# Optimization experiments

Hardware: AMD Instinct MI355X
Metric: run time of the kernel (lower is better)

The kernel has to match this reference:

```python
import jax, jax.numpy as jnp
import numpy as np

H = 1024
V = 50257
L = 512


def setup_inputs() -> dict:
    key = jax.random.key(0)
    ks = jax.random.split(key, 12)
    s = 0.02
    return {
        "input_tok": jax.random.randint(ks[0], (1,), 0, V, dtype=jnp.int64),
        "hidden": jax.random.normal(ks[1], (1, 1, H), dtype=jnp.float32),
        "encoder_outputs": jax.random.normal(ks[2], (L, 1, H), dtype=jnp.float32),
        "embedding_w": jax.random.normal(ks[3], (V, H), dtype=jnp.float32) * s,
        "attn_combine_w": jax.random.normal(ks[4], (H, 2 * H), dtype=jnp.float32) * s,
        "attn_combine_b": jax.random.normal(ks[5], (H,), dtype=jnp.float32) * s,
        "w_ih": jax.random.normal(ks[6], (3 * H, H), dtype=jnp.float32) * s,
        "w_hh": jax.random.normal(ks[7], (3 * H, H), dtype=jnp.float32) * s,
        "b_ih": jax.random.normal(ks[8], (3 * H,), dtype=jnp.float32) * s,
        "b_hh": jax.random.normal(ks[9], (3 * H,), dtype=jnp.float32) * s,
        "out_w": jax.random.normal(ks[10], (V, H), dtype=jnp.float32) * s,
        "out_b": jax.random.normal(ks[11], (V,), dtype=jnp.float32) * s,
    }


def reference(input_tok, hidden, encoder_outputs, embedding_w,
              attn_combine_w, attn_combine_b, w_ih, w_hh, b_ih, b_hh,
              out_w, out_b):
    # embedding(input).view(1,1,-1); dropout is identity in eval mode
    embedded = embedding_w[input_tok[0]][None, :]          # [1, H]
    enc = encoder_outputs[:, 0, :]                          # [L, H]
    h0 = hidden[0]                                          # [1, H]
    # dot-product attention: hidden[0] @ enc^T
    attn_weights = jax.nn.softmax(h0 @ enc.T, axis=1)      # [1, L]
    attn_applied = attn_weights @ enc                       # [1, H]
    combined = jnp.concatenate([embedded, attn_applied], axis=1)  # [1, 2H]
    x = jax.nn.relu(combined @ attn_combine_w.T + attn_combine_b)  # [1, H]
    # single-step GRU cell (PyTorch gate ordering: r, z, n)
    gi = x @ w_ih.T + b_ih                                  # [1, 3H]
    gh = h0 @ w_hh.T + b_hh                                 # [1, 3H]
    r = jax.nn.sigmoid(gi[:, :H] + gh[:, :H])
    z = jax.nn.sigmoid(gi[:, H:2 * H] + gh[:, H:2 * H])
    n = jnp.tanh(gi[:, 2 * H:] + r * gh[:, 2 * H:])
    h_new = (1.0 - z) * n + z * h0                          # [1, H]
    logp = jax.nn.log_softmax(h_new @ out_w.T + out_b, axis=1)  # [1, V]
    return logp, h_new[None], attn_weights
```

## Files before the change

kernel.cpp:

```cpp
#include <hip/hip_runtime.h>
#include <math.h>

#define H   1024
#define H2  2048
#define V   50257
#define L   512
#define NL  3142
#define NAB 16

__device__ __forceinline__ float dot4(float4 a, float4 b) {
    return a.x*b.x + a.y*b.y + a.z*b.z + a.w*b.w;
}
__device__ __forceinline__ float wave_red_sum(float v) {
    #pragma unroll
    for (int off = 32; off > 0; off >>= 1) v += __shfl_down(v, off, 64);
    return v;
}
__device__ __forceinline__ float wave_red_max(float v) {
    #pragma unroll
    for (int off = 32; off > 0; off >>= 1) v = fmaxf(v, __shfl_down(v, off, 64));
    return v;
}

__global__ void __launch_bounds__(256) k_scores(
        const float* __restrict__ h0, const float* __restrict__ enc,
        float* __restrict__ scores) {
    __shared__ float sred[4];
    int t = threadIdx.x, lane = t & 63, wv = t >> 6;
    int l = blockIdx.x;
    float4 a = ((const float4*)(enc + (size_t)l * H))[t];
    float4 b = ((const float4*)h0)[t];
    float acc = wave_red_sum(dot4(a, b));
    if (lane == 0) sred[wv] = acc;
    __syncthreads();
    if (t == 0) scores[l] = sred[0] + sred[1] + sred[2] + sred[3];
}

__global__ void __launch_bounds__(256) k_attn_part(
        const float* __restrict__ enc, const float* __restrict__ scores,
        float* __restrict__ partial, float* __restrict__ d_out) {
    __shared__ float wl[L];
    __shared__ float sred[4];
    int t = threadIdx.x, lane = t & 63, wv = t >> 6;
    float s0 = scores[t], s1 = scores[t + 256];
    float m = wave_red_max(fmaxf(s0, s1));
    if (lane == 0) sred[wv] = m;
    __syncthreads();
    float gmax = fmaxf(fmaxf(sred[0], sred[1]), fmaxf(sred[2], sred[3]));
    __syncthreads();
    float e0 = expf(s0 - gmax), e1 = expf(s1 - gmax);
    float ssum = wave_red_sum(e0 + e1);
    if (lane == 0) sred[wv] = ssum;
    __syncthreads();
    float inv = 1.f / (sred[0] + sred[1] + sred[2] + sred[3]);
    float w0 = e0 * inv, w1 = e1 * inv;
    wl[t] = w0; wl[t + 256] = w1;
    if (blockIdx.x == 0) {
        d_out[V + H + t]       = w0;
        d_out[V + H + 256 + t] = w1;
    }
    __syncthreads();
    int r0 = blockIdx.x * 32;
    float4 acc = make_float4(0.f, 0.f, 0.f, 0.f);
    #pragma unroll 8
    for (int k = 0; k < 32; ++k) {
        float w  = wl[r0 + k];
        float4 e = ((const float4*)(enc + (size_t)(r0 + k) * H))[t];
        acc.x += w * e.x; acc.y += w * e.y; acc.z += w * e.z; acc.w += w * e.w;
    }
    ((float4*)(partial + (size_t)blockIdx.x * H))[t] = acc;
}

__global__ void __launch_bounds__(256) k_combine(
        const float* __restrict__ emb_w, const int* __restrict__ tok,
        const float* __restrict__ partial, const float* __restrict__ Wc,
        const float* __restrict__ bc, float* __restrict__ x) {
    __shared__ float comb[H2];
    int t = threadIdx.x;
    float4 a = make_float4(0.f, 0.f, 0.f, 0.f);
    #pragma unroll
    for (int b = 0; b < NAB; ++b) {
        float4 p = ((const float4*)(partial + (size_t)b * H))[t];
        a.x += p.x; a.y += p.y; a.z += p.z; a.w += p.w;
    }
    int tk = tok[0];
    ((float4*)comb)[t]       = ((const float4*)(emb_w + (size_t)tk * H))[t];
    ((float4*)comb)[t + 256] = a;
    __syncthreads();
    int lane = t & 63, wv = t >> 6;
    int row = blockIdx.x * 4 + wv;
    const float4* wr = (const float4*)(Wc + (size_t)row * H2);
    float acc = 0.f;
    #pragma unroll
    for (int j = 0; j < 8; ++j)
        acc += dot4(wr[j * 64 + lane], ((const float4*)comb)[j * 64 + lane]);
    acc = wave_red_sum(acc);
    if (lane == 0) x[row] = fmaxf(acc + bc[row], 0.f);
}

__global__ void __launch_bounds__(256) k_gru(
        const float* __restrict__ x, const float* __restrict__ h0,
        const float* __restrict__ w_ih, const float* __restrict__ b_ih,
        const float* __restrict__ w_hh, const float* __restrict__ b_hh,
        float* __restrict__ d_out, float* __restrict__ hnew) {
    int t = threadIdx.x, lane = t & 63, wv = t >> 6;
    int i = blockIdx.x * 4 + wv;
    const float4* x4 = (const float4*)x;
    const float4* h4 = (const float4*)h0;
    const float4* wi0 = (const float4*)(w_ih + (size_t)i * H);
    const float4* wi1 = (const float4*)(w_ih + (size_t)(H + i) * H);
    const float4* wi2 = (const float4*)(w_ih + (size_t)(2 * H + i) * H);
    const float4* wh0 = (const float4*)(w_hh + (size_t)i * H);
    const float4* wh1 = (const float4*)(w_hh + (size_t)(H + i) * H);
    const float4* wh2 = (const float4*)(w_hh + (size_t)(2 * H + i) * H);
    float ai0 = 0.f, ai1 = 0.f, ai2 = 0.f, ah0 = 0.f, ah1 = 0.f, ah2 = 0.f;
    #pragma unroll
    for (int j = 0; j < 4; ++j) {
        int idx = j * 64 + lane;
        float4 xv = x4[idx], hv = h4[idx];
        ai0 += dot4(wi0[idx], xv);
        ai1 += dot4(wi1[idx], xv);
        ai2 += dot4(wi2[idx], xv);
        ah0 += dot4(wh0[idx], hv);
        ah1 += dot4(wh1[idx], hv);
        ah2 += dot4(wh2[idx], hv);
    }
    #pragma unroll
    for (int off = 32; off > 0; off >>= 1) {
        ai0 += __shfl_down(ai0, off, 64);
        ai1 += __shfl_down(ai1, off, 64);
        ai2 += __shfl_down(ai2, off, 64);
        ah0 += __shfl_down(ah0, off, 64);
        ah1 += __shfl_down(ah1, off, 64);
        ah2 += __shfl_down(ah2, off, 64);
    }
    if (lane == 0) {
        float r = 1.f / (1.f + expf(-(ai0 + b_ih[i]         + ah0 + b_hh[i])));
        float z = 1.f / (1.f + expf(-(ai1 + b_ih[H + i]     + ah1 + b_hh[H + i])));
        float n = tanhf(ai2 + b_ih[2 * H + i] + r * (ah2 + b_hh[2 * H + i]));
        float h = (1.f - z) * n + z * h0[i];
        d_out[V + i] = h;
        hnew[i] = h;
    }
}

__global__ void __launch_bounds__(256, 4) k_logits(
        const float* __restrict__ hnew, const float* __restrict__ out_w,
        const float* __restrict__ out_b, float* __restrict__ d_out,
        float* __restrict__ pm, float* __restrict__ ps) {
    __shared__ float sm[4], ss[4];
    int t = threadIdx.x, lane = t & 63, wv = t >> 6;
    int base = blockIdx.x * 16 + wv * 4;
    const float4* h4 = (const float4*)hnew;
    const float4* wr[4];
    #pragma unroll
    for (int r = 0; r < 4; ++r) {
        int row = (base + r < V) ? base + r : V - 1;
        wr[r] = (const float4*)(out_w + (size_t)row * H);
    }
    float a[4] = {0.f, 0.f, 0.f, 0.f};
    #pragma unroll
    for (int j = 0; j < 4; ++j) {
        float4 hv = h4[j * 64 + lane];
        #pragma unroll
        for (int r = 0; r < 4; ++r) a[r] += dot4(wr[r][j * 64 + lane], hv);
    }
    #pragma unroll
    for (int off = 32; off > 0; off >>= 1) {
        #pragma unroll
        for (int r = 0; r < 4; ++r) a[r] += __shfl_down(a[r], off, 64);
    }
    if (lane == 0) {
        float v[4];
        float m = -INFINITY;
        #pragma unroll
        for (int r = 0; r < 4; ++r) {
            int row = base + r;
            if (row < V) {
                v[r] = a[r] + out_b[row];
                d_out[row] = v[r];
                m = fmaxf(m, v[r]);
            } else v[r] = -INFINITY;
        }
        float s = 0.f;
        #pragma unroll
        for (int r = 0; r < 4; ++r)
            if (base + r < V) s += expf(v[r] - m);
        sm[wv] = m; ss[wv] = s;
    }
    __syncthreads();
    if (t == 0) {
        float M = fmaxf(fmaxf(sm[0], sm[1]), fmaxf(sm[2], sm[3]));
        float S = 0.f;
        #pragma unroll
        for (int k = 0; k < 4; ++k)
            if (sm[k] > -INFINITY) S += ss[k] * expf(sm[k] - M);
        pm[blockIdx.x] = M; ps[blockIdx.x] = S;
    }
}

__global__ void __launch_bounds__(256) k_logp(
        float* __restrict__ d_out, const float* __restrict__ pm,
        const float* __restrict__ ps) {
    __shared__ float sm[4], ss[4];
    int t = threadIdx.x, lane = t & 63, wv = t >> 6;
    float m = -INFINITY, s = 0.f;
    for (int i = t; i < NL; i += 256) {
        float mi = pm[i], si = ps[i];
        float mn = fmaxf(m, mi);
        s = s * expf(m - mn) + si * expf(mi - mn);
        m = mn;
    }
    #pragma unroll
    for (int off = 32; off > 0; off >>= 1) {
        float mo = __shfl_down(m, off, 64);
        float so = __shfl_down(s, off, 64);
        float mn = fmaxf(m, mo);
        s = s * expf(m - mn) + so * expf(mo - mn);
        m = mn;
    }
    if (lane == 0) { sm[wv] = m; ss[wv] = s; }
    __syncthreads();
    float M = fmaxf(fmaxf(sm[0], sm[1]), fmaxf(sm[2], sm[3]));
    float S = 0.f;
    #pragma unroll
    for (int k = 0; k < 4; ++k) S += ss[k] * expf(sm[k] - M);
    float off = M + logf(S);
    int i = blockIdx.x * 256 + t;
    if (i < V) d_out[i] -= off;
}

extern "C" void kernel_launch(void* const* d_in, const int* in_sizes, int n_in,
                              void* d_out, int out_size, void* d_ws, size_t ws_size,
                              hipStream_t stream) {
    const int*   tok    = (const int*)d_in[0];
    const float* hidden = (const float*)d_in[1];
    const float* enc    = (const float*)d_in[2];
    const float* emb_w  = (const float*)d_in[3];
    const float* Wc     = (const float*)d_in[4];
    const float* bc     = (const float*)d_in[5];
    const float* w_ih   = (const float*)d_in[6];
    const float* w_hh   = (const float*)d_in[7];
    const float* b_ih   = (const float*)d_in[8];
    const float* b_hh   = (const float*)d_in[9];
    const float* out_w  = (const float*)d_in[10];
    const float* out_b  = (const float*)d_in[11];
    float* out = (float*)d_out;
    float* ws  = (float*)d_ws;

    float* scores  = ws;
    float* partial = ws + 1024;
    float* xbuf    = ws + 17408;
    float* hnew    = ws + 18432;
    float* pm      = ws + 19456;
    float* psum    = ws + 23040;

    k_scores   <<<512, 256, 0, stream>>>(hidden, enc, scores);
    k_attn_part<<<NAB, 256, 0, stream>>>(enc, scores, partial, out);
    k_combine  <<<256, 256, 0, stream>>>(emb_w, tok, partial, Wc, bc, xbuf);
    k_gru      <<<256, 256, 0, stream>>>(xbuf, hidden, w_ih, b_ih, w_hh, b_hh, out, hnew);
    k_logits   <<<NL,  256, 0, stream>>>(hnew, out_w, out_b, out, pm, psum);
    k_logp     <<<(V + 255) / 256, 256, 0, stream>>>(out, pm, psum);
}
```

Before: 420.7 us.

## Fuse mid and output stages into persistent kernels with atomic grid barriers

Merges the attention-partial, combine and GRU kernels into one 256-block kernel separated by software grid barriers. It also merges the logits and log-softmax-normalise kernels into one 1024-block persistent kernel that loops over row groups with an online max/sum. This cuts launch count from six to three and the inter-kernel gaps. It relies on all blocks being co-resident for the spin barriers, which risks deadlock if occupancy does not allow it, and the barrier counters are reset by the first kernel.

```diff
diff --git a/kernel.cpp b/kernel.cpp
--- a/kernel.cpp
+++ b/kernel.cpp
@@ -5,8 +5,10 @@
 #define H2  2048
 #define V   50257
 #define L   512
-#define NL  3142
 #define NAB 16
+#define NB2 256
+#define NB3 1024
+#define NG3 3142
 
 __device__ __forceinline__ float dot4(float4 a, float4 b) {
     return a.x*b.x + a.y*b.y + a.z*b.z + a.w*b.w;
@@ -22,11 +24,24 @@
     return v;
 }
 
+__device__ __forceinline__ void grid_sync(int* cnt, int target) {
+    __syncthreads();
+    if (threadIdx.x == 0) {
+        __threadfence();
+        __hip_atomic_fetch_add(cnt, 1, __ATOMIC_ACQ_REL, __HIP_MEMORY_SCOPE_AGENT);
+        while (__hip_atomic_load(cnt, __ATOMIC_ACQUIRE, __HIP_MEMORY_SCOPE_AGENT) < target)
+            __builtin_amdgcn_s_sleep(2);
+        __threadfence();
+    }
+    __syncthreads();
+}
+
 __global__ void __launch_bounds__(256) k_scores(
         const float* __restrict__ h0, const float* __restrict__ enc,
-        float* __restrict__ scores) {
+        float* __restrict__ scores, int* __restrict__ cnt) {
     __shared__ float sred[4];
     int t = threadIdx.x, lane = t & 63, wv = t >> 6;
+    if (blockIdx.x == 0 && t < 8) cnt[t] = 0;
     int l = blockIdx.x;
     float4 a = ((const float4*)(enc + (size_t)l * H))[t];
     float4 b = ((const float4*)h0)[t];
@@ -36,198 +51,199 @@
     if (t == 0) scores[l] = sred[0] + sred[1] + sred[2] + sred[3];
 }
 
-__global__ void __launch_bounds__(256) k_attn_part(
+__global__ void __launch_bounds__(256) k_mid(
         const float* __restrict__ enc, const float* __restrict__ scores,
-        float* __restrict__ partial, float* __restrict__ d_out) {
-    __shared__ float wl[L];
-    __shared__ float sred[4];
-    int t = threadIdx.x, lane = t & 63, wv = t >> 6;
-    float s0 = scores[t], s1 = scores[t + 256];
-    float m = wave_red_max(fmaxf(s0, s1));
-    if (lane == 0) sred[wv] = m;
-    __syncthreads();
-    float gmax = fmaxf(fmaxf(sred[0], sred[1]), fmaxf(sred[2], sred[3]));
-    __syncthreads();
-    float e0 = expf(s0 - gmax), e1 = expf(s1 - gmax);
-    float ssum = wave_red_sum(e0 + e1);
-    if (lane == 0) sred[wv] = ssum;
-    __syncthreads();
-    float inv = 1.f / (sred[0] + sred[1] + sred[2] + sred[3]);
-    float w0 = e0 * inv, w1 = e1 * inv;
-    wl[t] = w0; wl[t + 256] = w1;
-    if (blockIdx.x == 0) {
-        d_out[V + H + t]       = w0;
-        d_out[V + H + 256 + t] = w1;
-    }
-    __syncthreads();
-    int r0 = blockIdx.x * 32;
-    float4 acc = make_float4(0.f, 0.f, 0.f, 0.f);
-    #pragma unroll 8
-    for (int k = 0; k < 32; ++k) {
-        float w  = wl[r0 + k];
-        float4 e = ((const float4*)(enc + (size_t)(r0 + k) * H))[t];
-        acc.x += w * e.x; acc.y += w * e.y; acc.z += w * e.z; acc.w += w * e.w;
-    }
-    ((float4*)(partial + (size_t)blockIdx.x * H))[t] = acc;
-}
-
-__global__ void __launch_bounds__(256) k_combine(
-        const float* __restrict__ emb_w, const int* __restrict__ tok,
-        const float* __restrict__ partial, const float* __restrict__ Wc,
-        const float* __restrict__ bc, float* __restrict__ x) {
-    __shared__ float comb[H2];
-    int t = threadIdx.x;
-    float4 a = make_float4(0.f, 0.f, 0.f, 0.f);
-    #pragma unroll
-    for (int b = 0; b < NAB; ++b) {
-        float4 p = ((const float4*)(partial + (size_t)b * H))[t];
-        a.x += p.x; a.y += p.y; a.z += p.z; a.w += p.w;
-    }
-    int tk = tok[0];
-    ((float4*)comb)[t]       = ((const float4*)(emb_w + (size_t)tk * H))[t];
-    ((float4*)comb)[t + 256] = a;
-    __syncthreads();
-    int lane = t & 63, wv = t >> 6;
-    int row = blockIdx.x * 4 + wv;
-    const float4* wr = (const float4*)(Wc + (size_t)row * H2);
-    float acc = 0.f;
-    #pragma unroll
-    for (int j = 0; j < 8; ++j)
-        acc += dot4(wr[j * 64 + lane], ((const float4*)comb)[j * 64 + lane]);
-    acc = wave_red_sum(acc);
-    if (lane == 0) x[row] = fmaxf(acc + bc[row], 0.f);
-}
-
-__global__ void __launch_bounds__(256) k_gru(
-        const float* __restrict__ x, const float* __restrict__ h0,
+        const int* __restrict__ tok, const float* __restrict__ emb_w,
+        const float* __restrict__ Wc, const float* __restrict__ bc,
         const float* __restrict__ w_ih, const float* __restrict__ b_ih,
         const float* __restrict__ w_hh, const float* __restrict__ b_hh,
-        float* __restrict__ d_out, float* __restrict__ hnew) {
-    int t = threadIdx.x, lane = t & 63, wv = t >> 6;
-    int i = blockIdx.x * 4 + wv;
-    const float4* x4 = (const float4*)x;
-    const float4* h4 = (const float4*)h0;
-    const float4* wi0 = (const float4*)(w_ih + (size_t)i * H);
-    const float4* wi1 = (const float4*)(w_ih + (size_t)(H + i) * H);
-    const float4* wi2 = (const float4*)(w_ih + (size_t)(2 * H + i) * H);
-    const float4* wh0 = (const float4*)(w_hh + (size_t)i * H);
-    const float4* wh1 = (const float4*)(w_hh + (size_t)(H + i) * H);
-    const float4* wh2 = (const float4*)(w_hh + (size_t)(2 * H + i) * H);
-    float ai0 = 0.f, ai1 = 0.f, ai2 = 0.f, ah0 = 0.f, ah1 = 0.f, ah2 = 0.f;
-    #pragma unroll
-    for (int j = 0; j < 4; ++j) {
-        int idx = j * 64 + lane;
-        float4 xv = x4[idx], hv = h4[idx];
-        ai0 += dot4(wi0[idx], xv);
-        ai1 += dot4(wi1[idx], xv);
-        ai2 += dot4(wi2[idx], xv);
-        ah0 += dot4(wh0[idx], hv);
-        ah1 += dot4(wh1[idx], hv);
-        ah2 += dot4(wh2[idx], hv);
-    }
-    #pragma unroll
-    for (int off = 32; off > 0; off >>= 1) {
-        ai0 += __shfl_down(ai0, off, 64);
-        ai1 += __shfl_down(ai1, off, 64);
-        ai2 += __shfl_down(ai2, off, 64);
-        ah0 += __shfl_down(ah0, off, 64);
-        ah1 += __shfl_down(ah1, off, 64);
-        ah2 += __shfl_down(ah2, off, 64);
-    }
-    if (lane == 0) {
-        float r = 1.f / (1.f + expf(-(ai0 + b_ih[i]         + ah0 + b_hh[i])));
-        float z = 1.f / (1.f + expf(-(ai1 + b_ih[H + i]     + ah1 + b_hh[H + i])));
-        float n = tanhf(ai2 + b_ih[2 * H + i] + r * (ah2 + b_hh[2 * H + i]));
-        float h = (1.f - z) * n + z * h0[i];
-        d_out[V + i] = h;
-        hnew[i] = h;
-    }
-}
-
-__global__ void __launch_bounds__(256, 4) k_logits(
+        const float* __restrict__ h0,
+        float* __restrict__ partial, float* __restrict__ xbuf,
+        float* __restrict__ hnew, float* __restrict__ d_out,
+        int* __restrict__ cnt) {
+    __shared__ float wl[L];
+    __shared__ float comb[H2];
+    __shared__ float sred[4];
+    int t = threadIdx.x, lane = t & 63, wv = t >> 6, b = blockIdx.x;
+
+    if (b < NAB) {
+        float s0 = scores[t], s1 = scores[t + 256];
+        float m = wave_red_max(fmaxf(s0, s1));
+        if (lane == 0) sred[wv] = m;
+        __syncthreads();
+        float gmax = fmaxf(fmaxf(sred[0], sred[1]), fmaxf(sred[2], sred[3]));
+        __syncthreads();
+        float e0 = expf(s0 - gmax), e1 = expf(s1 - gmax);
+        float ssum = wave_red_sum(e0 + e1);
+        if (lane == 0) sred[wv] = ssum;
+        __syncthreads();
+        float inv = 1.f / (sred[0] + sred[1] + sred[2] + sred[3]);
+        float w0 = e0 * inv, w1 = e1 * inv;
+        wl[t] = w0; wl[t + 256] = w1;
+        if (b == 0) {
+            d_out[V + H + t]       = w0;
+            d_out[V + H + 256 + t] = w1;
+        }
+        __syncthreads();
+        int r0 = b * 32;
+        float4 acc = make_float4(0.f, 0.f, 0.f, 0.f);
+        #pragma unroll 8
+        for (int k = 0; k < 32; ++k) {
+            float w  = wl[r0 + k];
+            float4 e = ((const float4*)(enc + (size_t)(r0 + k) * H))[t];
+            acc.x += w * e.x; acc.y += w * e.y; acc.z += w * e.z; acc.w += w * e.w;
+        }
+        ((float4*)(partial + (size_t)b * H))[t] = acc;
+    }
+    grid_sync(cnt + 0, NB2);
+
+    {
+        float4 a = make_float4(0.f, 0.f, 0.f, 0.f);
+        #pragma unroll
+        for (int p = 0; p < NAB; ++p) {
+            float4 q = ((const float4*)(partial + (size_t)p * H))[t];
+            a.x += q.x; a.y += q.y; a.z += q.z; a.w += q.w;
+        }
+        int tk = tok[0];
+        ((float4*)comb)[t]       = ((const float4*)(emb_w + (size_t)tk * H))[t];
+        ((float4*)comb)[t + 256] = a;
+        __syncthreads();
+        int row = b * 4 + wv;
+        const float4* wr = (const float4*)(Wc + (size_t)row * H2);
+        float acc = 0.f;
+        #pragma unroll
+        for (int j = 0; j < 8; ++j)
+            acc += dot4(wr[j * 64 + lane], ((const float4*)comb)[j * 64 + lane]);
+        acc = wave_red_sum(acc);
+        if (lane == 0) xbuf[row] = fmaxf(acc + bc[row], 0.f);
+    }
+    grid_sync(cnt + 1, NB2);
+
+    {
+        int i = b * 4 + wv;
+        const float4* x4 = (const float4*)xbuf;
+        const float4* h4 = (const float4*)h0;
+        const float4* wi0 = (const float4*)(w_ih + (size_t)i * H);
+        const float4* wi1 = (const float4*)(w_ih + (size_t)(H + i) * H);
+        const float4* wi2 = (const float4*)(w_ih + (size_t)(2 * H + i) * H);
+        const float4* wh0 = (const float4*)(w_hh + (size_t)i * H);
+        const float4* wh1 = (const float4*)(w_hh + (size_t)(H + i) * H);
+        const float4* wh2 = (const float4*)(w_hh + (size_t)(2 * H + i) * H);
+        float ai0 = 0.f, ai1 = 0.f, ai2 = 0.f, ah0 = 0.f, ah1 = 0.f, ah2 = 0.f;
+        #pragma unroll
+        for (int j = 0; j < 4; ++j) {
+            int idx = j * 64 + lane;
+            float4 xv = x4[idx], hv = h4[idx];
+            ai0 += dot4(wi0[idx], xv);
+            ai1 += dot4(wi1[idx], xv);
+            ai2 += dot4(wi2[idx], xv);
+            ah0 += dot4(wh0[idx], hv);
+            ah1 += dot4(wh1[idx], hv);
+            ah2 += dot4(wh2[idx], hv);
+        }
+        #pragma unroll
+        for (int off = 32; off > 0; off >>= 1) {
+            ai0 += __shfl_down(ai0, off, 64);
+            ai1 += __shfl_down(ai1, off, 64);
+            ai2 += __shfl_down(ai2, off, 64);
+            ah0 += __shfl_down(ah0, off, 64);
+            ah1 += __shfl_down(ah1, off, 64);
+            ah2 += __shfl_down(ah2, off, 64);
+        }
+        if (lane == 0) {
+            float r = 1.f / (1.f + expf(-(ai0 + b_ih[i]         + ah0 + b_hh[i])));
+            float z = 1.f / (1.f + expf(-(ai1 + b_ih[H + i]     + ah1 + b_hh[H + i])));
+            float n = tanhf(ai2 + b_ih[2 * H + i] + r * (ah2 + b_hh[2 * H + i]));
+            float h = (1.f - z) * n + z * h0[i];
+            d_out[V + i] = h;
+            hnew[i] = h;
+        }
+    }
+}
+
+__global__ void __launch_bounds__(256, 4) k_out(
         const float* __restrict__ hnew, const float* __restrict__ out_w,
         const float* __restrict__ out_b, float* __restrict__ d_out,
-        float* __restrict__ pm, float* __restrict__ ps) {
+        float* __restrict__ pm, float* __restrict__ ps,
+        int* __restrict__ cnt) {
     __shared__ float sm[4], ss[4];
-    int t = threadIdx.x, lane = t & 63, wv = t >> 6;
-    int base = blockIdx.x * 16 + wv * 4;
+    int t = threadIdx.x, lane = t & 63, wv = t >> 6, b = blockIdx.x;
     const float4* h4 = (const float4*)hnew;
-    const float4* wr[4];
-    #pragma unroll
-    for (int r = 0; r < 4; ++r) {
-        int row = (base + r < V) ? base + r : V - 1;
-        wr[r] = (const float4*)(out_w + (size_t)row * H);
-    }
-    float a[4] = {0.f, 0.f, 0.f, 0.f};
-    #pragma unroll
-    for (int j = 0; j < 4; ++j) {
-        float4 hv = h4[j * 64 + lane];
-        #pragma unroll
-        for (int r = 0; r < 4; ++r) a[r] += dot4(wr[r][j * 64 + lane], hv);
-    }
-    #pragma unroll
-    for (int off = 32; off > 0; off >>= 1) {
-        #pragma unroll
-        for (int r = 0; r < 4; ++r) a[r] += __shfl_down(a[r], off, 64);
-    }
-    if (lane == 0) {
-        float v[4];
-        float m = -INFINITY;
+
+    float m_run = -INFINITY, s_run = 0.f;
+    for (int g = b; g < NG3; g += NB3) {
+        int base = g * 16 + wv * 4;
+        const float4* wr[4];
         #pragma unroll
         for (int r = 0; r < 4; ++r) {
-            int row = base + r;
-            if (row < V) {
-                v[r] = a[r] + out_b[row];
-                d_out[row] = v[r];
-                m = fmaxf(m, v[r]);
-            } else v[r] = -INFINITY;
-        }
-        float s = 0.f;
-        #pragma unroll
-        for (int r = 0; r < 4; ++r)
-            if (base + r < V) s += expf(v[r] - m);
-        sm[wv] = m; ss[wv] = s;
-    }
+            int row = (base + r < V) ? base + r : V - 1;
+            wr[r] = (const float4*)(out_w + (size_t)row * H);
+        }
+        float a[4] = {0.f, 0.f, 0.f, 0.f};
+        #pragma unroll
+        for (int j = 0; j < 4; ++j) {
+            float4 hv = h4[j * 64 + lane];
+            #pragma unroll
+            for (int r = 0; r < 4; ++r) a[r] += dot4(wr[r][j * 64 + lane], hv);
+        }
+        #pragma unroll
+        for (int off = 32; off > 0; off >>= 1) {
+            #pragma unroll
+            for (int r = 0; r < 4; ++r) a[r] += __shfl_down(a[r], off, 64);
+        }
+        if (lane == 0) {
+            #pragma unroll
+            for (int r = 0; r < 4; ++r) {
+                int row = base + r;
+                if (row < V) {
+                    float v = a[r] + out_b[row];
+                    d_out[row] = v;
+                    float mn = fmaxf(m_run, v);
+                    s_run = s_run * expf(m_run - mn) + expf(v - mn);
+                    m_run = mn;
+                }
+            }
+        }
+    }
+    if (lane == 0) { sm[wv] = m_run; ss[wv] = s_run; }
     __syncthreads();
     if (t == 0) {
         float M = fmaxf(fmaxf(sm[0], sm[1]), fmaxf(sm[2], sm[3]));
         float S = 0.f;
         #pragma unroll
-        for (int k = 0; k < 4; ++k)
-            if (sm[k] > -INFINITY) S += ss[k] * expf(sm[k] - M);
-        pm[blockIdx.x] = M; ps[blockIdx.x] = S;
-    }
-}
-
-__global__ void __launch_bounds__(256) k_logp(
-        float* __restrict__ d_out, const float* __restrict__ pm,
-        const float* __restrict__ ps) {
-    __shared__ float sm[4], ss[4];
-    int t = threadIdx.x, lane = t & 63, wv = t >> 6;
-    float m = -INFINITY, s = 0.f;
-    for (int i = t; i < NL; i += 256) {
-        float mi = pm[i], si = ps[i];
-        float mn = fmaxf(m, mi);
-        s = s * expf(m - mn) + si * expf(mi - mn);
-        m = mn;
-    }
-    #pragma unroll
-    for (int off = 32; off > 0; off >>= 1) {
-        float mo = __shfl_down(m, off, 64);
-        float so = __shfl_down(s, off, 64);
-        float mn = fmaxf(m, mo);
-        s = s * expf(m - mn) + so * expf(mo - mn);
-        m = mn;
-    }
-    if (lane == 0) { sm[wv] = m; ss[wv] = s; }
-    __syncthreads();
-    float M = fmaxf(fmaxf(sm[0], sm[1]), fmaxf(sm[2], sm[3]));
-    float S = 0.f;
-    #pragma unroll
-    for (int k = 0; k < 4; ++k) S += ss[k] * expf(sm[k] - M);
-    float off = M + logf(S);
-    int i = blockIdx.x * 256 + t;
-    if (i < V) d_out[i] -= off;
+        for (int k = 0; k < 4; ++k) S += ss[k] * expf(sm[k] - M);
+        pm[b] = M; ps[b] = S;
+    }
+    grid_sync(cnt + 2, NB3);
+
+    {
+        float m = -INFINITY, s = 0.f;
+        #pragma unroll
+        for (int k = 0; k < 4; ++k) {
+            int i = t * 4 + k;
+            float mi = pm[i], si = ps[i];
+            float mn = fmaxf(m, mi);
+            s = s * expf(m - mn) + si * expf(mi - mn);
+            m = mn;
+        }
+        #pragma unroll
+        for (int off = 32; off > 0; off >>= 1) {
+            float mo = __shfl_down(m, off, 64);
+            float so = __shfl_down(s, off, 64);
+            float mn = fmaxf(m, mo);
+            s = s * expf(m - mn) + so * expf(mo - mn);
+            m = mn;
+        }
+        if (lane == 0) { sm[wv] = m; ss[wv] = s; }
+        __syncthreads();
+        float M = fmaxf(fmaxf(sm[0], sm[1]), fmaxf(sm[2], sm[3]));
+        float S = 0.f;
+        #pragma unroll
+        for (int k = 0; k < 4; ++k) S += ss[k] * expf(sm[k] - M);
+        float off = M + logf(S);
+        int i = b * 256 + t;
+        if (i < V) d_out[i] -= off;
+    }
 }
 
 extern "C" void kernel_launch(void* const* d_in, const int* in_sizes, int n_in,
@@ -253,12 +269,12 @@
     float* xbuf    = ws + 17408;
     float* hnew    = ws + 18432;
     float* pm      = ws + 19456;
-    float* psum    = ws + 23040;
-
-    k_scores   <<<512, 256, 0, stream>>>(hidden, enc, scores);
-    k_attn_part<<<NAB, 256, 0, stream>>>(enc, scores, partial, out);
-    k_combine  <<<256, 256, 0, stream>>>(emb_w, tok, partial, Wc, bc, xbuf);
-    k_gru      <<<256, 256, 0, stream>>>(xbuf, hidden, w_ih, b_ih, w_hh, b_hh, out, hnew);
-    k_logits   <<<NL,  256, 0, stream>>>(hnew, out_w, out_b, out, pm, psum);
-    k_logp     <<<(V + 255) / 256, 256, 0, stream>>>(out, pm, psum);
-}
+    float* psum    = ws + 20480;
+    int*   cnt     = (int*)(ws + 21504);
+
+    k_scores<<<512, 256, 0, stream>>>(hidden, enc, scores, cnt);
+    k_mid   <<<NB2, 256, 0, stream>>>(enc, scores, tok, emb_w, Wc, bc,
+                                      w_ih, b_ih, w_hh, b_hh, hidden,
+                                      partial, xbuf, hnew, out, cnt);
+    k_out   <<<NB3, 256, 0, stream>>>(hnew, out_w, out_b, out, pm, psum, cnt);
+}
```

New measurement: 637.8 us. 51.6% more time.
